# Performance work log

Hardware: AMD Instinct MI355X
Metric: run time of the kernel (lower is better)

The kernel has to match this reference:

```python
import jax, jax.numpy as jnp
import numpy as np

B, N, QDIM, KVDIM, DIM, H = 2, 4096, 256, 256, 256, 8


def setup_inputs() -> dict:
    key = jax.random.key(0)
    ks = jax.random.split(key, 8)
    s = 0.02
    return {
        "x": jax.random.normal(ks[0], (B, N, QDIM), jnp.float32),
        "y": jax.random.normal(ks[1], (B, N, KVDIM), jnp.float32),
        "Wq": jax.random.normal(ks[2], (DIM, QDIM), jnp.float32) * s,
        "bq": jnp.zeros((DIM,), jnp.float32),
        "Wk": jax.random.normal(ks[3], (DIM, KVDIM), jnp.float32) * s,
        "bk": jnp.zeros((DIM,), jnp.float32),
        "Wv": jax.random.normal(ks[4], (DIM, KVDIM), jnp.float32) * s,
        "bv": jnp.zeros((DIM,), jnp.float32),
        "Wo": jax.random.normal(ks[5], (DIM, DIM), jnp.float32) * s,
        "bo": jnp.zeros((DIM,), jnp.float32),
    }


def reference(x, y, Wq, bq, Wk, bk, Wv, bv, Wo, bo):
    b, n, _ = x.shape
    h = H
    scale = KVDIM ** (-0.5)  # note: full kv_dim, as in the source
    q = x @ Wq.T + bq  # (b, n, dim)
    k = y @ Wk.T + bk
    v = y @ Wv.T + bv
    def split(t):
        return t.reshape(b, -1, h, DIM // h).transpose(0, 2, 1, 3)  # b h n d
    q, k, v = split(q), split(k), split(v)
    dots = jnp.einsum('bhid,bhjd->bhij', q, k) * scale
    attn = jax.nn.softmax(dots, axis=-1)
    out = jnp.einsum('bhij,bhjd->bhid', attn, v)
    out = out.transpose(0, 2, 1, 3).reshape(b, n, DIM)  # b n (h d)
    out = out @ Wo.T + bo
    return out
```

## Files before the change

### kernel.cpp

```cpp
#include <hip/hip_runtime.h>

#define BATCH 2
#define SEQ   4096
#define DIM   256
#define NHEAD 8
#define HDIM  32
#define ROWS  (BATCH * SEQ)

typedef __attribute__((ext_vector_type(8))) short short8;
typedef __attribute__((ext_vector_type(8))) unsigned short ushort8;
typedef __attribute__((ext_vector_type(4))) unsigned short ushortx4;
typedef __attribute__((ext_vector_type(4))) float floatx4;
typedef __attribute__((ext_vector_type(2))) unsigned int uintx2;
typedef __attribute__((ext_vector_type(4))) unsigned int uintx4;

static __device__ __forceinline__ unsigned short f2bf(float f) {
    union { float f; unsigned u; } v; v.f = f;
    unsigned r = v.u + 0x7fffu + ((v.u >> 16) & 1u);
    return (unsigned short)(r >> 16);
}
static __device__ __forceinline__ unsigned fbits(float f) {
    union { float f; unsigned u; } v; v.f = f; return v.u;
}
static __device__ __forceinline__ unsigned pack2(float a, float b) {
    return __builtin_amdgcn_perm(fbits(b), fbits(a), 0x07060302u);
}
static __device__ __forceinline__ void g2l16(const void* g, void* l) {
    __builtin_amdgcn_global_load_lds(
        (const __attribute__((address_space(1))) unsigned int*)g,
        (__attribute__((address_space(3))) unsigned int*)l, 16, 0, 0);
}

#if __has_builtin(__builtin_amdgcn_permlane32_swap) && __has_builtin(__builtin_amdgcn_permlane16_swap)
#define HAVE_PLSWAP 1
#else
#define HAVE_PLSWAP 0
#endif

__global__ __launch_bounds__(256) void convw_kernel(
    const float* __restrict__ W0, const float* __restrict__ W1,
    const float* __restrict__ W2, const float* __restrict__ W3,
    unsigned short* __restrict__ o0, unsigned short* __restrict__ o1,
    unsigned short* __restrict__ o2, unsigned short* __restrict__ o3) {
    const float* s; unsigned short* d;
    switch (blockIdx.y) {
        case 0:  s = W0; d = o0; break;
        case 1:  s = W1; d = o1; break;
        case 2:  s = W2; d = o2; break;
        default: s = W3; d = o3; break;
    }
    long off = ((long)blockIdx.x * 256 + threadIdx.x) * 4;
    float4 v = *(const float4*)(s + off);
    ushortx4 o;
    o.x = f2bf(v.x); o.y = f2bf(v.y); o.z = f2bf(v.z); o.w = f2bf(v.w);
    *(ushortx4*)(d + off) = o;
}

__global__ __launch_bounds__(256, 2) void qkv_kernel(
    const float* __restrict__ x, const float* __restrict__ y,
    const unsigned short* __restrict__ Wq, const unsigned short* __restrict__ Wk,
    const unsigned short* __restrict__ Wv,
    const float* __restrict__ bq, const float* __restrict__ bk, const float* __restrict__ bv,
    unsigned short* __restrict__ qo, unsigned short* __restrict__ ko,
    unsigned short* __restrict__ vto) {
    __shared__ unsigned short Abuf[8][64][32];
    const int tid = threadIdx.x, lane = tid & 63, wave = tid >> 6;
    const int ql = lane & 15, quad = lane >> 4;
    const int mat = blockIdx.y;
    const int m0 = blockIdx.x * 64;
    const float* A = (mat == 0) ? x : y;
    const unsigned short* W = (mat == 0) ? Wq : (mat == 1) ? Wk : Wv;
    const float* bias = (mat == 0) ? bq : (mat == 1) ? bk : bv;

    {
        const int row = tid >> 2, c8 = (tid & 3) * 8;
        const int swz = ((tid & 3) ^ ((row >> 1) & 3)) * 8;
        const float* src = A + (long)(m0 + row) * DIM + c8;
#pragma unroll
        for (int kb = 0; kb < 8; kb++) {
            float4 v0 = *(const float4*)(src + kb * 32);
            float4 v1 = *(const float4*)(src + kb * 32 + 4);
            ushort8 o;
            o[0] = f2bf(v0.x); o[1] = f2bf(v0.y); o[2] = f2bf(v0.z); o[3] = f2bf(v0.w);
            o[4] = f2bf(v1.x); o[5] = f2bf(v1.y); o[6] = f2bf(v1.z); o[7] = f2bf(v1.w);
            *(ushort8*)(&Abuf[kb][row][swz]) = o;
        }
    }
    __syncthreads();
    const int n0 = wave * 64;
    const int akey = (quad ^ ((ql >> 1) & 3)) * 8;
    floatx4 acc[4][4] = {};
#pragma unroll
    for (int kb = 0; kb < 8; kb++) {
        short8 wf[4], af[4];
#pragma unroll
        for (int u = 0; u < 4; u++)
            wf[u] = *(const short8*)(W + (long)(n0 + u*16 + ql) * DIM + kb*32 + quad*8);
#pragma unroll
        for (int t = 0; t < 4; t++)
            af[t] = *(const short8*)(&Abuf[kb][t*16 + ql][akey]);
        if (mat < 2) {
#pragma unroll
            for (int t = 0; t < 4; t++)
#pragma unroll
                for (int u = 0; u < 4; u++)
                    acc[t][u] = __builtin_amdgcn_mfma_f32_16x16x32_bf16(wf[u], af[t], acc[t][u], 0, 0, 0);
        } else {
#pragma unroll
            for (int t = 0; t < 4; t++)
#pragma unroll
                for (int u = 0; u < 4; u++)
                    acc[t][u] = __builtin_amdgcn_mfma_f32_16x16x32_bf16(af[t], wf[u], acc[t][u], 0, 0, 0);
        }
    }
    if (mat < 2) {
        const float scale = (mat == 0) ? 0.09016844005556021f : 1.0f;
        unsigned short* out = (mat == 0) ? qo : ko;
#pragma unroll
        for (int t = 0; t < 4; t++) {
            int m = m0 + t*16 + ql;
#pragma unroll
            for (int u = 0; u < 4; u++) {
                int n = n0 + u*16 + quad*4;
                float4 b4 = *(const float4*)(bias + n);
                ushortx4 o;
                o.x = f2bf((acc[t][u][0] + b4.x) * scale);
                o.y = f2bf((acc[t][u][1] + b4.y) * scale);
                o.z = f2bf((acc[t][u][2] + b4.z) * scale);
                o.w = f2bf((acc[t][u][3] + b4.w) * scale);
                *(ushortx4*)(out + (long)m * DIM + n) = o;
            }
        }
    } else {
#pragma unroll
        for (int t = 0; t < 4; t++) {
            int mb = m0 + t*16 + quad*4;
            int bi = mb >> 12, i0 = mb & (SEQ - 1);
#pragma unroll
            for (int u = 0; u < 4; u++) {
                int n = n0 + u*16 + ql;
                float b = bias[n];
                ushortx4 o;
                o.x = f2bf(acc[t][u][0] + b);
                o.y = f2bf(acc[t][u][1] + b);
                o.z = f2bf(acc[t][u][2] + b);
                o.w = f2bf(acc[t][u][3] + b);
                *(ushortx4*)(vto + ((long)(bi * DIM + n)) * SEQ + i0) = o;
            }
        }
    }
}

template<int NSPLIT>
__global__ __launch_bounds__(256, 4) void attn_kernel(
    const unsigned short* __restrict__ qb, const unsigned short* __restrict__ kbuf,
    const unsigned short* __restrict__ vT,
    float* __restrict__ opart, float* __restrict__ lbuf) {
    __shared__ unsigned short K0[64 * 32], K1[64 * 32];
    __shared__ unsigned short V0[32 * 64], V1[32 * 64];
#if !HAVE_PLSWAP
    __shared__ unsigned short P[4][32][72];
#endif
    const int tid = threadIdx.x, lane = tid & 63, wave = tid >> 6;
    const int ql = lane & 15, quad = lane >> 4;
    const int bh = blockIdx.y, b = bh >> 3, h = bh & 7;
    const int part = blockIdx.z;
    const int kvb = part * (SEQ / NSPLIT);
    const int q0 = blockIdx.x * 128 + wave * 32;

    const unsigned short* qrow = qb   + (long)b * SEQ * DIM + h * HDIM;
    const unsigned short* krow = kbuf + (long)b * SEQ * DIM + h * HDIM;
    const unsigned short* vrow = vT   + (long)(b * DIM + h * HDIM) * SEQ;

    short8 qf[2];
#pragma unroll
    for (int t = 0; t < 2; t++)
        qf[t] = *(const short8*)(qrow + (long)(q0 + t*16 + ql) * DIM + quad*8);

    short8 ones;
#pragma unroll
    for (int i = 0; i < 8; i++) ones[i] = (short)0x3F80;

    const unsigned short* kg = krow + (long)(kvb + wave*16 + (lane >> 2)) * DIM
                                    + ((lane & 3) ^ ((lane >> 3) & 3)) * 8;
    const unsigned short* vg = vrow + (long)(wave*8 + (lane >> 3)) * SEQ + kvb
                                    + ((lane & 7) ^ (lane >> 3)) * 8;
    unsigned short* kd0 = K0 + wave * 512;  unsigned short* kd1 = K1 + wave * 512;
    unsigned short* vd0 = V0 + wave * 512;  unsigned short* vd1 = V1 + wave * 512;
    const int kro = (quad ^ ((ql >> 1) & 3)) * 8;
    const int vmask = ql & 7;

    floatx4 acc[2][2] = {};
    floatx4 accL[2] = {};

    auto compute = [&](const unsigned short* Ks, const unsigned short* Vs) {
        unsigned pk[4][2][2];
#pragma unroll
        for (int mt = 0; mt < 4; ++mt) {
            short8 kf = *(const short8*)(Ks + (mt*16 + ql) * 32 + kro);
#pragma unroll
            for (int t = 0; t < 2; t++) {
                floatx4 z = {};
                floatx4 s = __builtin_amdgcn_mfma_f32_16x16x32_bf16(kf, qf[t], z, 0, 0, 0);
                float p0 = __builtin_amdgcn_exp2f(s[0]);
                float p1 = __builtin_amdgcn_exp2f(s[1]);
                float p2 = __builtin_amdgcn_exp2f(s[2]);
                float p3 = __builtin_amdgcn_exp2f(s[3]);
                pk[mt][t][0] = pack2(p0, p1);
                pk[mt][t][1] = pack2(p2, p3);
#if !HAVE_PLSWAP
                uintx2 w; w.x = pk[mt][t][0]; w.y = pk[mt][t][1];
                *(uintx2*)(&P[wave][t*16 + ql][mt*16 + quad*4]) = w;
#endif
            }
        }
#pragma unroll
        for (int ks = 0; ks < 2; ++ks) {
            short8 pf[2];
#pragma unroll
            for (int t = 0; t < 2; t++) {
#if HAVE_PLSWAP
                uintx2 x0 = __builtin_amdgcn_permlane32_swap(pk[2*ks][t][0], pk[2*ks+1][t][0], false, false);
                uintx2 y0 = __builtin_amdgcn_permlane16_swap(x0.x, x0.y, false, false);
                uintx2 x1 = __builtin_amdgcn_permlane32_swap(pk[2*ks][t][1], pk[2*ks+1][t][1], false, false);
                uintx2 y1 = __builtin_amdgcn_permlane16_swap(x1.x, x1.y, false, false);
                uintx4 pv; pv.x = y0.x; pv.y = y1.x; pv.z = y0.y; pv.w = y1.y;
                pf[t] = *(short8*)&pv;
#else
                pf[t] = *(const short8*)(&P[wave][t*16 + ql][ks*32 + quad*8]);
#endif
            }
#pragma unroll
            for (int t = 0; t < 2; t++)
                accL[t] = __builtin_amdgcn_mfma_f32_16x16x32_bf16(ones, pf[t], accL[t], 0, 0, 0);
#pragma unroll
            for (int dt = 0; dt < 2; ++dt) {
                short8 vf = *(const short8*)(Vs + (dt*16 + ql) * 64 + ((ks*4 + quad) ^ vmask) * 8);
#pragma unroll
                for (int t = 0; t < 2; t++)
                    acc[dt][t] = __builtin_amdgcn_mfma_f32_16x16x32_bf16(vf, pf[t], acc[dt][t], 0, 0, 0);
            }
        }
    };

    g2l16(kg, kd0); g2l16(vg, vd0);
    __syncthreads();
    const int NIT = SEQ / 64 / NSPLIT;
    for (int it = 0; it < NIT; it += 2) {
        if (it + 1 < NIT) {
            g2l16(kg + (long)(it + 1) * 64 * DIM, kd1);
            g2l16(vg + (it + 1) * 64, vd1);
        }
        compute(K0, V0);
        __syncthreads();
        if (it + 2 < NIT) {
            g2l16(kg + (long)(it + 2) * 64 * DIM, kd0);
            g2l16(vg + (it + 2) * 64, vd0);
        }
        compute(K1, V1);
        __syncthreads();
    }

    float* obase = opart + (long)part * ROWS * DIM;
#pragma unroll
    for (int dt = 0; dt < 2; dt++)
#pragma unroll
        for (int t = 0; t < 2; t++) {
            float4 o;
            o.x = acc[dt][t][0]; o.y = acc[dt][t][1];
            o.z = acc[dt][t][2]; o.w = acc[dt][t][3];
            *(float4*)(obase + (long)(b*SEQ + q0 + t*16 + ql) * DIM + h*HDIM + dt*16 + quad*4) = o;
        }
    if (quad == 0) {
#pragma unroll
        for (int t = 0; t < 2; t++)
            lbuf[(long)(part * NHEAD + h) * ROWS + b*SEQ + q0 + t*16 + ql] = accL[t][0];
    }
}

template<int NSPLIT>
__global__ __launch_bounds__(256, 2) void oproj_kernel(
    const float* __restrict__ opart, const float* __restrict__ lbuf,
    const unsigned short* __restrict__ W, const float* __restrict__ bias,
    float* __restrict__ out) {
    __shared__ unsigned short Abuf[8][64][32];
    const int tid = threadIdx.x, lane = tid & 63, wave = tid >> 6;
    const int ql = lane & 15, quad = lane >> 4;
    const int m0 = blockIdx.x * 64;

    {
        const int row = tid >> 2, c8 = (tid & 3) * 8;
        const int swz = ((tid & 3) ^ ((row >> 1) & 3)) * 8;
        const float* s0 = opart + (long)(m0 + row) * DIM + c8;
#pragma unroll
        for (int kb = 0; kb < 8; kb++) {
            float li = 0.f;
#pragma unroll
            for (int i = 0; i < NSPLIT; i++)
                li += lbuf[(long)(i * NHEAD + kb) * ROWS + m0 + row];
            float r = __builtin_amdgcn_rcpf(li);
            float a[8] = {};
#pragma unroll
            for (int i = 0; i < NSPLIT; i++) {
                const float* si = s0 + (long)i * ROWS * DIM;
                float4 a0 = *(const float4*)(si + kb * 32);
                float4 a1 = *(const float4*)(si + kb * 32 + 4);
                a[0] += a0.x; a[1] += a0.y; a[2] += a0.z; a[3] += a0.w;
                a[4] += a1.x; a[5] += a1.y; a[6] += a1.z; a[7] += a1.w;
            }
            ushort8 o;
#pragma unroll
            for (int e = 0; e < 8; e++) o[e] = f2bf(a[e] * r);
            *(ushort8*)(&Abuf[kb][row][swz]) = o;
        }
    }
    __syncthreads();
    const int n0 = wave * 64;
    const int akey = (quad ^ ((ql >> 1) & 3)) * 8;
    floatx4 acc[4][4] = {};
#pragma unroll
    for (int kb = 0; kb < 8; kb++) {
        short8 wf[4], af[4];
#pragma unroll
        for (int u = 0; u < 4; u++)
            wf[u] = *(const short8*)(W + (long)(n0 + u*16 + ql) * DIM + kb*32 + quad*8);
#pragma unroll
        for (int t = 0; t < 4; t++)
            af[t] = *(const short8*)(&Abuf[kb][t*16 + ql][akey]);
#pragma unroll
        for (int t = 0; t < 4; t++)
#pragma unroll
            for (int u = 0; u < 4; u++)
                acc[t][u] = __builtin_amdgcn_mfma_f32_16x16x32_bf16(wf[u], af[t], acc[t][u], 0, 0, 0);
    }
#pragma unroll
    for (int t = 0; t < 4; t++) {
        int m = m0 + t*16 + ql;
#pragma unroll
        for (int u = 0; u < 4; u++) {
            int n = n0 + u*16 + quad*4;
            float4 b4 = *(const float4*)(bias + n);
            float4 o;
            o.x = acc[t][u][0] + b4.x;
            o.y = acc[t][u][1] + b4.y;
            o.z = acc[t][u][2] + b4.z;
            o.w = acc[t][u][3] + b4.w;
            *(float4*)(out + (long)m * DIM + n) = o;
        }
    }
}

extern "C" void kernel_launch(void* const* d_in, const int* in_sizes, int n_in,
                              void* d_out, int out_size, void* d_ws, size_t ws_size,
                              hipStream_t stream) {
    const float* x  = (const float*)d_in[0];
    const float* y  = (const float*)d_in[1];
    const float* Wq = (const float*)d_in[2];
    const float* bq = (const float*)d_in[3];
    const float* Wk = (const float*)d_in[4];
    const float* bk = (const float*)d_in[5];
    const float* Wv = (const float*)d_in[6];
    const float* bv = (const float*)d_in[7];
    const float* Wo = (const float*)d_in[8];
    const float* bo = (const float*)d_in[9];
    float* out = (float*)d_out;

    const long NX = (long)ROWS * DIM;
    const long NW = (long)DIM * DIM;
    unsigned short* Wqb  = (unsigned short*)d_ws;
    unsigned short* Wkb  = Wqb + NW;
    unsigned short* Wvb  = Wkb + NW;
    unsigned short* Wob  = Wvb + NW;
    unsigned short* qbf  = Wob + NW;
    unsigned short* kbf  = qbf + NX;
    unsigned short* vTb  = kbf + NX;
    float* opart = (float*)(vTb + NX);
    const size_t base = (size_t)(4*NW + 3*NX) * 2;
    const size_t need4 = base + (size_t)(4*NX + 4*NHEAD*ROWS) * 4;

    convw_kernel<<<dim3(NW / 1024, 4), dim3(256), 0, stream>>>(
        Wq, Wk, Wv, Wo, Wqb, Wkb, Wvb, Wob);

    qkv_kernel<<<dim3(ROWS / 64, 3), dim3(256), 0, stream>>>(
        x, y, Wqb, Wkb, Wvb, bq, bk, bv, qbf, kbf, vTb);

    if (ws_size >= need4) {
        float* lbuf = opart + 4 * NX;
        attn_kernel<4><<<dim3(SEQ / 128, BATCH * NHEAD, 4), dim3(256), 0, stream>>>(
            qbf, kbf, vTb, opart, lbuf);
        oproj_kernel<4><<<dim3(ROWS / 64), dim3(256), 0, stream>>>(
            opart, lbuf, Wob, bo, out);
    } else {
        float* lbuf = opart + 2 * NX;
        attn_kernel<2><<<dim3(SEQ / 128, BATCH * NHEAD, 2), dim3(256), 0, stream>>>(
            qbf, kbf, vTb, opart, lbuf);
        oproj_kernel<2><<<dim3(ROWS / 64), dim3(256), 0, stream>>>(
            opart, lbuf, Wob, bo, out);
    }
}
```

Measured before the change: 154.2 us.

## Give each attention wave 64 queries with private double-buffered K/V tiles

The attention kernel moves from 256-thread to 128-thread blocks. Each wave now owns 64 query rows and stages its own 32-key K/V tiles into per-wave double buffers, so the block-wide __syncthreads between tiles go away and each K/V fragment is reused across four query tiles instead of two. The KV step shrinks from 64 to 32 keys and the V swizzle changes to match. In exchange, every wave fetches the full K/V stream itself, duplicating global loads within a block. Correctness now relies on the per-wave loads completing before compute without a barrier, and the kernel uses more registers for the larger accumulators.

```diff
diff --git a/kernel.cpp b/kernel.cpp
--- a/kernel.cpp
+++ b/kernel.cpp
@@ -152,54 +152,60 @@
 }
 
 template<int NSPLIT>
-__global__ __launch_bounds__(256, 4) void attn_kernel(
+__global__ __launch_bounds__(128, 4) void attn_kernel(
     const unsigned short* __restrict__ qb, const unsigned short* __restrict__ kbuf,
     const unsigned short* __restrict__ vT,
     float* __restrict__ opart, float* __restrict__ lbuf) {
-    __shared__ unsigned short K0[64 * 32], K1[64 * 32];
-    __shared__ unsigned short V0[32 * 64], V1[32 * 64];
+    __shared__ unsigned short KA[2][1024], KB[2][1024];
+    __shared__ unsigned short VA[2][1024], VB[2][1024];
 #if !HAVE_PLSWAP
-    __shared__ unsigned short P[4][32][72];
+    __shared__ unsigned short P[2][64][40];
 #endif
     const int tid = threadIdx.x, lane = tid & 63, wave = tid >> 6;
     const int ql = lane & 15, quad = lane >> 4;
     const int bh = blockIdx.y, b = bh >> 3, h = bh & 7;
     const int part = blockIdx.z;
     const int kvb = part * (SEQ / NSPLIT);
-    const int q0 = blockIdx.x * 128 + wave * 32;
+    const int q0 = blockIdx.x * 128 + wave * 64;
 
     const unsigned short* qrow = qb   + (long)b * SEQ * DIM + h * HDIM;
     const unsigned short* krow = kbuf + (long)b * SEQ * DIM + h * HDIM;
     const unsigned short* vrow = vT   + (long)(b * DIM + h * HDIM) * SEQ;
 
-    short8 qf[2];
-#pragma unroll
-    for (int t = 0; t < 2; t++)
+    short8 qf[4];
+#pragma unroll
+    for (int t = 0; t < 4; t++)
         qf[t] = *(const short8*)(qrow + (long)(q0 + t*16 + ql) * DIM + quad*8);
 
     short8 ones;
 #pragma unroll
     for (int i = 0; i < 8; i++) ones[i] = (short)0x3F80;
 
-    const unsigned short* kg = krow + (long)(kvb + wave*16 + (lane >> 2)) * DIM
+    const unsigned short* kg = krow + (long)(kvb + (lane >> 2)) * DIM
                                     + ((lane & 3) ^ ((lane >> 3) & 3)) * 8;
-    const unsigned short* vg = vrow + (long)(wave*8 + (lane >> 3)) * SEQ + kvb
-                                    + ((lane & 7) ^ (lane >> 3)) * 8;
-    unsigned short* kd0 = K0 + wave * 512;  unsigned short* kd1 = K1 + wave * 512;
-    unsigned short* vd0 = V0 + wave * 512;  unsigned short* vd1 = V1 + wave * 512;
+    const unsigned short* vg = vrow + (long)(lane >> 2) * SEQ + kvb
+                                    + ((lane & 3) ^ ((lane >> 2) & 3)) * 8;
+    unsigned short* ka = KA[wave]; unsigned short* kb2 = KB[wave];
+    unsigned short* va = VA[wave]; unsigned short* vb = VB[wave];
     const int kro = (quad ^ ((ql >> 1) & 3)) * 8;
-    const int vmask = ql & 7;
-
-    floatx4 acc[2][2] = {};
-    floatx4 accL[2] = {};
-
+    const int vro = 0;
+
+    floatx4 acc[2][4] = {};
+    floatx4 accL[4] = {};
+
+    auto stage = [&](unsigned short* Kd, unsigned short* Vd, int kv0) {
+        g2l16(kg + (long)kv0 * DIM, Kd);
+        g2l16(kg + (long)(kv0 + 16) * DIM, Kd + 512);
+        g2l16(vg + kv0, Vd);
+        g2l16(vg + (long)16 * SEQ + kv0, Vd + 512);
+    };
     auto compute = [&](const unsigned short* Ks, const unsigned short* Vs) {
-        unsigned pk[4][2][2];
-#pragma unroll
-        for (int mt = 0; mt < 4; ++mt) {
+        unsigned pk[2][4][2];
+#pragma unroll
+        for (int mt = 0; mt < 2; ++mt) {
             short8 kf = *(const short8*)(Ks + (mt*16 + ql) * 32 + kro);
 #pragma unroll
-            for (int t = 0; t < 2; t++) {
+            for (int t = 0; t < 4; t++) {
                 floatx4 z = {};
                 floatx4 s = __builtin_amdgcn_mfma_f32_16x16x32_bf16(kf, qf[t], z, 0, 0, 0);
                 float p0 = __builtin_amdgcn_exp2f(s[0]);
@@ -214,58 +220,45 @@
 #endif
             }
         }
-#pragma unroll
-        for (int ks = 0; ks < 2; ++ks) {
-            short8 pf[2];
-#pragma unroll
-            for (int t = 0; t < 2; t++) {
+        short8 pf[4];
+#pragma unroll
+        for (int t = 0; t < 4; t++) {
 #if HAVE_PLSWAP
-                uintx2 x0 = __builtin_amdgcn_permlane32_swap(pk[2*ks][t][0], pk[2*ks+1][t][0], false, false);
-                uintx2 y0 = __builtin_amdgcn_permlane16_swap(x0.x, x0.y, false, false);
-                uintx2 x1 = __builtin_amdgcn_permlane32_swap(pk[2*ks][t][1], pk[2*ks+1][t][1], false, false);
-                uintx2 y1 = __builtin_amdgcn_permlane16_swap(x1.x, x1.y, false, false);
-                uintx4 pv; pv.x = y0.x; pv.y = y1.x; pv.z = y0.y; pv.w = y1.y;
-                pf[t] = *(short8*)&pv;
+            uintx2 x0 = __builtin_amdgcn_permlane32_swap(pk[0][t][0], pk[1][t][0], false, false);
+            uintx2 y0 = __builtin_amdgcn_permlane16_swap(x0.x, x0.y, false, false);
+            uintx2 x1 = __builtin_amdgcn_permlane32_swap(pk[0][t][1], pk[1][t][1], false, false);
+            uintx2 y1 = __builtin_amdgcn_permlane16_swap(x1.x, x1.y, false, false);
+            uintx4 pv; pv.x = y0.x; pv.y = y1.x; pv.z = y0.y; pv.w = y1.y;
+            pf[t] = *(short8*)&pv;
 #else
-                pf[t] = *(const short8*)(&P[wave][t*16 + ql][ks*32 + quad*8]);
+            pf[t] = *(const short8*)(&P[wave][t*16 + ql][quad*8]);
 #endif
-            }
-#pragma unroll
-            for (int t = 0; t < 2; t++)
-                accL[t] = __builtin_amdgcn_mfma_f32_16x16x32_bf16(ones, pf[t], accL[t], 0, 0, 0);
-#pragma unroll
-            for (int dt = 0; dt < 2; ++dt) {
-                short8 vf = *(const short8*)(Vs + (dt*16 + ql) * 64 + ((ks*4 + quad) ^ vmask) * 8);
-#pragma unroll
-                for (int t = 0; t < 2; t++)
-                    acc[dt][t] = __builtin_amdgcn_mfma_f32_16x16x32_bf16(vf, pf[t], acc[dt][t], 0, 0, 0);
-            }
+            accL[t] = __builtin_amdgcn_mfma_f32_16x16x32_bf16(ones, pf[t], accL[t], 0, 0, 0);
+        }
+#pragma unroll
+        for (int dt = 0; dt < 2; ++dt) {
+            short8 vf = *(const short8*)(Vs + (dt*16 + ql) * 32 + ((quad ^ (ql & 3)) * 8));
+#pragma unroll
+            for (int t = 0; t < 4; t++)
+                acc[dt][t] = __builtin_amdgcn_mfma_f32_16x16x32_bf16(vf, pf[t], acc[dt][t], 0, 0, 0);
         }
     };
 
-    g2l16(kg, kd0); g2l16(vg, vd0);
-    __syncthreads();
-    const int NIT = SEQ / 64 / NSPLIT;
+    const int NIT = SEQ / 32 / NSPLIT;
+    stage(ka, va, 0);
+    stage(kb2, vb, 32);
     for (int it = 0; it < NIT; it += 2) {
-        if (it + 1 < NIT) {
-            g2l16(kg + (long)(it + 1) * 64 * DIM, kd1);
-            g2l16(vg + (it + 1) * 64, vd1);
-        }
-        compute(K0, V0);
-        __syncthreads();
-        if (it + 2 < NIT) {
-            g2l16(kg + (long)(it + 2) * 64 * DIM, kd0);
-            g2l16(vg + (it + 2) * 64, vd0);
-        }
-        compute(K1, V1);
-        __syncthreads();
+        compute(ka, va);
+        if (it + 2 < NIT) stage(ka, va, (it + 2) * 32);
+        compute(kb2, vb);
+        if (it + 3 < NIT) stage(kb2, vb, (it + 3) * 32);
     }
 
     float* obase = opart + (long)part * ROWS * DIM;
 #pragma unroll
     for (int dt = 0; dt < 2; dt++)
 #pragma unroll
-        for (int t = 0; t < 2; t++) {
+        for (int t = 0; t < 4; t++) {
             float4 o;
             o.x = acc[dt][t][0]; o.y = acc[dt][t][1];
             o.z = acc[dt][t][2]; o.w = acc[dt][t][3];
@@ -273,7 +266,7 @@
         }
     if (quad == 0) {
 #pragma unroll
-        for (int t = 0; t < 2; t++)
+        for (int t = 0; t < 4; t++)
             lbuf[(long)(part * NHEAD + h) * ROWS + b*SEQ + q0 + t*16 + ql] = accL[t][0];
     }
 }
@@ -386,13 +379,13 @@
 
     if (ws_size >= need4) {
         float* lbuf = opart + 4 * NX;
-        attn_kernel<4><<<dim3(SEQ / 128, BATCH * NHEAD, 4), dim3(256), 0, stream>>>(
+        attn_kernel<4><<<dim3(SEQ / 128, BATCH * NHEAD, 4), dim3(128), 0, stream>>>(
             qbf, kbf, vTb, opart, lbuf);
         oproj_kernel<4><<<dim3(ROWS / 64), dim3(256), 0, stream>>>(
             opart, lbuf, Wob, bo, out);
     } else {
         float* lbuf = opart + 2 * NX;
-        attn_kernel<2><<<dim3(SEQ / 128, BATCH * NHEAD, 2), dim3(256), 0, stream>>>(
+        attn_kernel<2><<<dim3(SEQ / 128, BATCH * NHEAD, 2), dim3(128), 0, stream>>>(
             qbf, kbf, vTb, opart, lbuf);
         oproj_kernel<2><<<dim3(ROWS / 64), dim3(256), 0, stream>>>(
             opart, lbuf, Wob, bo, out);
```

Result: slower. 161.7 us (+4.8%).

## Retile QKV and oproj grids and double attention KV tile to 128

Applied to the files above, without the earlier changes.

The QKV projection splits each 64-row block across two 128-column halves, giving twice as many blocks with smaller per-wave accumulators. The attention kernel now stages 128 keys per iteration (two 64-key halves per compute call), halving barriers and loop iterations at the cost of doubled LDS for the K/V buffers. The output projection uses 32-row blocks with one thread per row-head pair for the split reduction. Together these aim for more parallelism and fewer syncs, but add LDS pressure that may lower attention occupancy.

```diff
diff --git a/kernel.cpp b/kernel.cpp
--- a/kernel.cpp
+++ b/kernel.cpp
@@ -66,8 +66,10 @@
     __shared__ unsigned short Abuf[8][64][32];
     const int tid = threadIdx.x, lane = tid & 63, wave = tid >> 6;
     const int ql = lane & 15, quad = lane >> 4;
-    const int mat = blockIdx.y;
+    const int wm = wave >> 1, wn = wave & 1;
+    const int mat = blockIdx.z;
     const int m0 = blockIdx.x * 64;
+    const int nb = blockIdx.y * 128;
     const float* A = (mat == 0) ? x : y;
     const unsigned short* W = (mat == 0) ? Wq : (mat == 1) ? Wk : Wv;
     const float* bias = (mat == 0) ? bq : (mat == 1) ? bk : bv;
@@ -87,27 +89,27 @@
         }
     }
     __syncthreads();
-    const int n0 = wave * 64;
+    const int n0 = nb + wn * 64;
     const int akey = (quad ^ ((ql >> 1) & 3)) * 8;
-    floatx4 acc[4][4] = {};
+    floatx4 acc[2][4] = {};
 #pragma unroll
     for (int kb = 0; kb < 8; kb++) {
-        short8 wf[4], af[4];
+        short8 wf[4], af[2];
 #pragma unroll
         for (int u = 0; u < 4; u++)
             wf[u] = *(const short8*)(W + (long)(n0 + u*16 + ql) * DIM + kb*32 + quad*8);
 #pragma unroll
-        for (int t = 0; t < 4; t++)
-            af[t] = *(const short8*)(&Abuf[kb][t*16 + ql][akey]);
+        for (int t = 0; t < 2; t++)
+            af[t] = *(const short8*)(&Abuf[kb][wm*32 + t*16 + ql][akey]);
         if (mat < 2) {
 #pragma unroll
-            for (int t = 0; t < 4; t++)
+            for (int t = 0; t < 2; t++)
 #pragma unroll
                 for (int u = 0; u < 4; u++)
                     acc[t][u] = __builtin_amdgcn_mfma_f32_16x16x32_bf16(wf[u], af[t], acc[t][u], 0, 0, 0);
         } else {
 #pragma unroll
-            for (int t = 0; t < 4; t++)
+            for (int t = 0; t < 2; t++)
 #pragma unroll
                 for (int u = 0; u < 4; u++)
                     acc[t][u] = __builtin_amdgcn_mfma_f32_16x16x32_bf16(af[t], wf[u], acc[t][u], 0, 0, 0);
@@ -117,8 +119,8 @@
         const float scale = (mat == 0) ? 0.09016844005556021f : 1.0f;
         unsigned short* out = (mat == 0) ? qo : ko;
 #pragma unroll
-        for (int t = 0; t < 4; t++) {
-            int m = m0 + t*16 + ql;
+        for (int t = 0; t < 2; t++) {
+            int m = m0 + wm*32 + t*16 + ql;
 #pragma unroll
             for (int u = 0; u < 4; u++) {
                 int n = n0 + u*16 + quad*4;
@@ -133,8 +135,8 @@
         }
     } else {
 #pragma unroll
-        for (int t = 0; t < 4; t++) {
-            int mb = m0 + t*16 + quad*4;
+        for (int t = 0; t < 2; t++) {
+            int mb = m0 + wm*32 + t*16 + quad*4;
             int bi = mb >> 12, i0 = mb & (SEQ - 1);
 #pragma unroll
             for (int u = 0; u < 4; u++) {
@@ -156,8 +158,8 @@
     const unsigned short* __restrict__ qb, const unsigned short* __restrict__ kbuf,
     const unsigned short* __restrict__ vT,
     float* __restrict__ opart, float* __restrict__ lbuf) {
-    __shared__ unsigned short K0[64 * 32], K1[64 * 32];
-    __shared__ unsigned short V0[32 * 64], V1[32 * 64];
+    __shared__ unsigned short K0[128 * 32], K1[128 * 32];
+    __shared__ unsigned short V0[32 * 128], V1[32 * 128];
 #if !HAVE_PLSWAP
     __shared__ unsigned short P[4][32][72];
 #endif
@@ -181,82 +183,88 @@
 #pragma unroll
     for (int i = 0; i < 8; i++) ones[i] = (short)0x3F80;
 
-    const unsigned short* kg = krow + (long)(kvb + wave*16 + (lane >> 2)) * DIM
-                                    + ((lane & 3) ^ ((lane >> 3) & 3)) * 8;
-    const unsigned short* vg = vrow + (long)(wave*8 + (lane >> 3)) * SEQ + kvb
-                                    + ((lane & 7) ^ (lane >> 3)) * 8;
-    unsigned short* kd0 = K0 + wave * 512;  unsigned short* kd1 = K1 + wave * 512;
-    unsigned short* vd0 = V0 + wave * 512;  unsigned short* vd1 = V1 + wave * 512;
+    const int kc0 = wave * 2, kc1 = wave * 2 + 1;
+    const int klr = lane >> 2, kswz = ((lane & 3) ^ ((lane >> 3) & 3)) * 8;
+    const unsigned short* kg0 = krow + (long)(kvb + kc0*16 + klr) * DIM + kswz;
+    const unsigned short* kg1 = krow + (long)(kvb + kc1*16 + klr) * DIM + kswz;
+    const int vlr = lane >> 4, vcl = lane & 15;
+    const int vsw0 = (vcl ^ ((kc0*4 + vlr) & 7)) * 8;
+    const int vsw1 = (vcl ^ ((kc1*4 + vlr) & 7)) * 8;
+    const unsigned short* vg0 = vrow + (long)(kc0*4 + vlr) * SEQ + kvb + vsw0;
+    const unsigned short* vg1 = vrow + (long)(kc1*4 + vlr) * SEQ + kvb + vsw1;
+
     const int kro = (quad ^ ((ql >> 1) & 3)) * 8;
     const int vmask = ql & 7;
 
     floatx4 acc[2][2] = {};
     floatx4 accL[2] = {};
 
+    auto stage = [&](unsigned short* Kd, unsigned short* Vd, int kv0) {
+        g2l16(kg0 + (long)kv0 * DIM, Kd + kc0 * 512);
+        g2l16(kg1 + (long)kv0 * DIM, Kd + kc1 * 512);
+        g2l16(vg0 + kv0, Vd + kc0 * 512);
+        g2l16(vg1 + kv0, Vd + kc1 * 512);
+    };
     auto compute = [&](const unsigned short* Ks, const unsigned short* Vs) {
-        unsigned pk[4][2][2];
-#pragma unroll
-        for (int mt = 0; mt < 4; ++mt) {
-            short8 kf = *(const short8*)(Ks + (mt*16 + ql) * 32 + kro);
-#pragma unroll
-            for (int t = 0; t < 2; t++) {
-                floatx4 z = {};
-                floatx4 s = __builtin_amdgcn_mfma_f32_16x16x32_bf16(kf, qf[t], z, 0, 0, 0);
-                float p0 = __builtin_amdgcn_exp2f(s[0]);
-                float p1 = __builtin_amdgcn_exp2f(s[1]);
-                float p2 = __builtin_amdgcn_exp2f(s[2]);
-                float p3 = __builtin_amdgcn_exp2f(s[3]);
-                pk[mt][t][0] = pack2(p0, p1);
-                pk[mt][t][1] = pack2(p2, p3);
+#pragma unroll
+        for (int half = 0; half < 2; ++half) {
+            unsigned pk[4][2][2];
+#pragma unroll
+            for (int mt = 0; mt < 4; ++mt) {
+                short8 kf = *(const short8*)(Ks + (half*64 + mt*16 + ql) * 32 + kro);
+#pragma unroll
+                for (int t = 0; t < 2; t++) {
+                    floatx4 z = {};
+                    floatx4 s = __builtin_amdgcn_mfma_f32_16x16x32_bf16(kf, qf[t], z, 0, 0, 0);
+                    float p0 = __builtin_amdgcn_exp2f(s[0]);
+                    float p1 = __builtin_amdgcn_exp2f(s[1]);
+                    float p2 = __builtin_amdgcn_exp2f(s[2]);
+                    float p3 = __builtin_amdgcn_exp2f(s[3]);
+                    pk[mt][t][0] = pack2(p0, p1);
+                    pk[mt][t][1] = pack2(p2, p3);
 #if !HAVE_PLSWAP
-                uintx2 w; w.x = pk[mt][t][0]; w.y = pk[mt][t][1];
-                *(uintx2*)(&P[wave][t*16 + ql][mt*16 + quad*4]) = w;
+                    uintx2 w; w.x = pk[mt][t][0]; w.y = pk[mt][t][1];
+                    *(uintx2*)(&P[wave][t*16 + ql][mt*16 + quad*4]) = w;
 #endif
+                }
             }
-        }
-#pragma unroll
-        for (int ks = 0; ks < 2; ++ks) {
-            short8 pf[2];
-#pragma unroll
-            for (int t = 0; t < 2; t++) {
+#pragma unroll
+            for (int ks = 0; ks < 2; ++ks) {
+                short8 pf[2];
+#pragma unroll
+                for (int t = 0; t < 2; t++) {
 #if HAVE_PLSWAP
-                uintx2 x0 = __builtin_amdgcn_permlane32_swap(pk[2*ks][t][0], pk[2*ks+1][t][0], false, false);
-                uintx2 y0 = __builtin_amdgcn_permlane16_swap(x0.x, x0.y, false, false);
-                uintx2 x1 = __builtin_amdgcn_permlane32_swap(pk[2*ks][t][1], pk[2*ks+1][t][1], false, false);
-                uintx2 y1 = __builtin_amdgcn_permlane16_swap(x1.x, x1.y, false, false);
-                uintx4 pv; pv.x = y0.x; pv.y = y1.x; pv.z = y0.y; pv.w = y1.y;
-                pf[t] = *(short8*)&pv;
+                    uintx2 x0 = __builtin_amdgcn_permlane32_swap(pk[2*ks][t][0], pk[2*ks+1][t][0], false, false);
+                    uintx2 y0 = __builtin_amdgcn_permlane16_swap(x0.x, x0.y, false, false);
+                    uintx2 x1 = __builtin_amdgcn_permlane32_swap(pk[2*ks][t][1], pk[2*ks+1][t][1], false, false);
+                    uintx2 y1 = __builtin_amdgcn_permlane16_swap(x1.x, x1.y, false, false);
+                    uintx4 pv; pv.x = y0.x; pv.y = y1.x; pv.z = y0.y; pv.w = y1.y;
+                    pf[t] = *(short8*)&pv;
 #else
-                pf[t] = *(const short8*)(&P[wave][t*16 + ql][ks*32 + quad*8]);
+                    pf[t] = *(const short8*)(&P[wave][t*16 + ql][ks*32 + quad*8]);
 #endif
+                    accL[t] = __builtin_amdgcn_mfma_f32_16x16x32_bf16(ones, pf[t], accL[t], 0, 0, 0);
+                }
+#pragma unroll
+                for (int dt = 0; dt < 2; ++dt) {
+                    int vco = ((8*half + 4*ks + quad) ^ vmask) * 8;
+                    short8 vf = *(const short8*)(Vs + (dt*16 + ql) * 128 + vco);
+#pragma unroll
+                    for (int t = 0; t < 2; t++)
+                        acc[dt][t] = __builtin_amdgcn_mfma_f32_16x16x32_bf16(vf, pf[t], acc[dt][t], 0, 0, 0);
+                }
             }
-#pragma unroll
-            for (int t = 0; t < 2; t++)
-                accL[t] = __builtin_amdgcn_mfma_f32_16x16x32_bf16(ones, pf[t], accL[t], 0, 0, 0);
-#pragma unroll
-            for (int dt = 0; dt < 2; ++dt) {
-                short8 vf = *(const short8*)(Vs + (dt*16 + ql) * 64 + ((ks*4 + quad) ^ vmask) * 8);
-#pragma unroll
-                for (int t = 0; t < 2; t++)
-                    acc[dt][t] = __builtin_amdgcn_mfma_f32_16x16x32_bf16(vf, pf[t], acc[dt][t], 0, 0, 0);
-            }
         }
     };
 
-    g2l16(kg, kd0); g2l16(vg, vd0);
+    const int NIT = SEQ / 128 / NSPLIT;
+    stage(K0, V0, 0);
     __syncthreads();
-    const int NIT = SEQ / 64 / NSPLIT;
     for (int it = 0; it < NIT; it += 2) {
-        if (it + 1 < NIT) {
-            g2l16(kg + (long)(it + 1) * 64 * DIM, kd1);
-            g2l16(vg + (it + 1) * 64, vd1);
-        }
+        if (it + 1 < NIT) stage(K1, V1, (it + 1) * 128);
         compute(K0, V0);
         __syncthreads();
-        if (it + 2 < NIT) {
-            g2l16(kg + (long)(it + 2) * 64 * DIM, kd0);
-            g2l16(vg + (it + 2) * 64, vd0);
-        }
+        if (it + 2 < NIT) stage(K0, V0, (it + 2) * 128);
         compute(K1, V1);
         __syncthreads();
     }
@@ -283,58 +291,59 @@
     const float* __restrict__ opart, const float* __restrict__ lbuf,
     const unsigned short* __restrict__ W, const float* __restrict__ bias,
     float* __restrict__ out) {
-    __shared__ unsigned short Abuf[8][64][32];
+    __shared__ unsigned short Abuf[8][32][32];
     const int tid = threadIdx.x, lane = tid & 63, wave = tid >> 6;
     const int ql = lane & 15, quad = lane >> 4;
-    const int m0 = blockIdx.x * 64;
+    const int m0 = blockIdx.x * 32;
 
     {
-        const int row = tid >> 2, c8 = (tid & 3) * 8;
-        const int swz = ((tid & 3) ^ ((row >> 1) & 3)) * 8;
-        const float* s0 = opart + (long)(m0 + row) * DIM + c8;
-#pragma unroll
-        for (int kb = 0; kb < 8; kb++) {
-            float li = 0.f;
-#pragma unroll
-            for (int i = 0; i < NSPLIT; i++)
-                li += lbuf[(long)(i * NHEAD + kb) * ROWS + m0 + row];
-            float r = __builtin_amdgcn_rcpf(li);
-            float a[8] = {};
-#pragma unroll
-            for (int i = 0; i < NSPLIT; i++) {
-                const float* si = s0 + (long)i * ROWS * DIM;
-                float4 a0 = *(const float4*)(si + kb * 32);
-                float4 a1 = *(const float4*)(si + kb * 32 + 4);
-                a[0] += a0.x; a[1] += a0.y; a[2] += a0.z; a[3] += a0.w;
-                a[4] += a1.x; a[5] += a1.y; a[6] += a1.z; a[7] += a1.w;
+        const int row = tid >> 3, kb = tid & 7;
+        float li = 0.f;
+#pragma unroll
+        for (int i = 0; i < NSPLIT; i++)
+            li += lbuf[(long)(i * NHEAD + kb) * ROWS + m0 + row];
+        float r = __builtin_amdgcn_rcpf(li);
+        const float* s0 = opart + (long)(m0 + row) * DIM + kb * 32;
+        float a[32] = {};
+#pragma unroll
+        for (int i = 0; i < NSPLIT; i++) {
+            const float* si = s0 + (long)i * ROWS * DIM;
+#pragma unroll
+            for (int c = 0; c < 8; c++) {
+                float4 v = *(const float4*)(si + c * 4);
+                a[c*4+0] += v.x; a[c*4+1] += v.y; a[c*4+2] += v.z; a[c*4+3] += v.w;
             }
+        }
+        const int key = (row >> 1) & 3;
+#pragma unroll
+        for (int c2 = 0; c2 < 4; c2++) {
             ushort8 o;
 #pragma unroll
-            for (int e = 0; e < 8; e++) o[e] = f2bf(a[e] * r);
-            *(ushort8*)(&Abuf[kb][row][swz]) = o;
+            for (int e = 0; e < 8; e++) o[e] = f2bf(a[c2*8 + e] * r);
+            *(ushort8*)(&Abuf[kb][row][(c2 ^ key) * 8]) = o;
         }
     }
     __syncthreads();
     const int n0 = wave * 64;
     const int akey = (quad ^ ((ql >> 1) & 3)) * 8;
-    floatx4 acc[4][4] = {};
+    floatx4 acc[2][4] = {};
 #pragma unroll
     for (int kb = 0; kb < 8; kb++) {
-        short8 wf[4], af[4];
+        short8 wf[4], af[2];
 #pragma unroll
         for (int u = 0; u < 4; u++)
             wf[u] = *(const short8*)(W + (long)(n0 + u*16 + ql) * DIM + kb*32 + quad*8);
 #pragma unroll
-        for (int t = 0; t < 4; t++)
+        for (int t = 0; t < 2; t++)
             af[t] = *(const short8*)(&Abuf[kb][t*16 + ql][akey]);
 #pragma unroll
-        for (int t = 0; t < 4; t++)
+        for (int t = 0; t < 2; t++)
 #pragma unroll
             for (int u = 0; u < 4; u++)
                 acc[t][u] = __builtin_amdgcn_mfma_f32_16x16x32_bf16(wf[u], af[t], acc[t][u], 0, 0, 0);
     }
 #pragma unroll
-    for (int t = 0; t < 4; t++) {
+    for (int t = 0; t < 2; t++) {
         int m = m0 + t*16 + ql;
 #pragma unroll
         for (int u = 0; u < 4; u++) {
@@ -381,20 +390,20 @@
     convw_kernel<<<dim3(NW / 1024, 4), dim3(256), 0, stream>>>(
         Wq, Wk, Wv, Wo, Wqb, Wkb, Wvb, Wob);
 
-    qkv_kernel<<<dim3(ROWS / 64, 3), dim3(256), 0, stream>>>(
+    qkv_kernel<<<dim3(ROWS / 64, 2, 3), dim3(256), 0, stream>>>(
         x, y, Wqb, Wkb, Wvb, bq, bk, bv, qbf, kbf, vTb);
 
     if (ws_size >= need4) {
         float* lbuf = opart + 4 * NX;
         attn_kernel<4><<<dim3(SEQ / 128, BATCH * NHEAD, 4), dim3(256), 0, stream>>>(
             qbf, kbf, vTb, opart, lbuf);
-        oproj_kernel<4><<<dim3(ROWS / 64), dim3(256), 0, stream>>>(
+        oproj_kernel<4><<<dim3(ROWS / 32), dim3(256), 0, stream>>>(
             opart, lbuf, Wob, bo, out);
     } else {
         float* lbuf = opart + 2 * NX;
         attn_kernel<2><<<dim3(SEQ / 128, BATCH * NHEAD, 2), dim3(256), 0, stream>>>(
             qbf, kbf, vTb, opart, lbuf);
-        oproj_kernel<2><<<dim3(ROWS / 64), dim3(256), 0, stream>>>(
+        oproj_kernel<2><<<dim3(ROWS / 32), dim3(256), 0, stream>>>(
             opart, lbuf, Wob, bo, out);
     }
 }
```

New measurement: 162.0 us. 5.1% more time.
